# Kernel optimization log

Hardware: AMD Instinct MI355X
Metric: run time of the kernel (lower is better)

Reference implementation:

```python
import jax, jax.numpy as jnp
import numpy as np

EMBED_DIM = 1024
NUM_HEADS = 16
HEAD_DIM = EMBED_DIM // NUM_HEADS


def setup_inputs() -> dict:
    key = jax.random.key(0)
    kx, kw1, kb1, kw2, kb2 = jax.random.split(key, 5)
    B, T, C = 4, 2048, EMBED_DIM
    s = 1.0 / np.sqrt(C)
    return {
        "x": jax.random.normal(kx, (B, T, C), dtype=jnp.float32),
        "qkv_w": jax.random.normal(kw1, (3 * C, C), dtype=jnp.float32) * s,
        "qkv_b": jax.random.normal(kb1, (3 * C,), dtype=jnp.float32) * 0.01,
        "proj_w": jax.random.normal(kw2, (C, C), dtype=jnp.float32) * s,
        "proj_b": jax.random.normal(kb2, (C,), dtype=jnp.float32) * 0.01,
    }


def reference(x, qkv_w, qkv_b, proj_w, proj_b):
    B, T, C = x.shape
    H, D = NUM_HEADS, HEAD_DIM
    qkv = jnp.einsum('btc,oc->bto', x, qkv_w) + qkv_b  # [B,T,3C]
    q, k, v = jnp.split(qkv, 3, axis=-1)
    def heads(t):
        return t.reshape(B, T, H, D).transpose(0, 2, 1, 3)  # [B,H,T,D]
    q, k, v = heads(q), heads(k), heads(v)
    scale = 1.0 / jnp.sqrt(jnp.asarray(D, dtype=x.dtype))
    att = jnp.einsum('bhqd,bhkd->bhqk', q, k) * scale  # [B,H,T,T]
    causal = jnp.tril(jnp.ones((T, T), dtype=bool))
    att = jnp.where(causal, att, -jnp.inf)
    att = jax.nn.softmax(att, axis=-1)
    out = jnp.einsum('bhqk,bhkd->bhqd', att, v)  # [B,H,T,D]
    out = out.transpose(0, 2, 1, 3).reshape(B, T, C)
    out = jnp.einsum('btc,oc->bto', out, proj_w) + proj_b
    return out
```

## Files before the change

### kernel.cpp

```cpp
#include <hip/hip_runtime.h>
#include <hip/hip_bf16.h>

typedef __bf16 bf16x8 __attribute__((ext_vector_type(8)));
typedef __bf16 bf16x4 __attribute__((ext_vector_type(4)));
typedef float  f32x4  __attribute__((ext_vector_type(4)));

#define MFMA16(a, b, c) __builtin_amdgcn_mfma_f32_16x16x32_bf16((a), (b), (c), 0, 0, 0)
#define GLD16(g, l)                                                              \
    __builtin_amdgcn_global_load_lds(                                            \
        (const __attribute__((address_space(1))) void*)(g),                      \
        (__attribute__((address_space(3))) void*)(l), 16, 0, 0)

__global__ __launch_bounds__(256) void cvt3_f32_bf16(const float* __restrict__ a, __bf16* __restrict__ oa, int na,
                                                     const float* __restrict__ b, __bf16* __restrict__ ob, int nb,
                                                     const float* __restrict__ c, __bf16* __restrict__ oc, int nc) {
    const int stride = gridDim.x * blockDim.x * 4;
    const int start = (blockIdx.x * blockDim.x + threadIdx.x) * 4;
    for (int i = start; i < na; i += stride) {
        float4 v = *(const float4*)(a + i);
        bf16x4 o; o[0] = (__bf16)v.x; o[1] = (__bf16)v.y; o[2] = (__bf16)v.z; o[3] = (__bf16)v.w;
        *(bf16x4*)(oa + i) = o;
    }
    for (int i = start; i < nb; i += stride) {
        float4 v = *(const float4*)(b + i);
        bf16x4 o; o[0] = (__bf16)v.x; o[1] = (__bf16)v.y; o[2] = (__bf16)v.z; o[3] = (__bf16)v.w;
        *(bf16x4*)(ob + i) = o;
    }
    for (int i = start; i < nc; i += stride) {
        float4 v = *(const float4*)(c + i);
        bf16x4 o; o[0] = (__bf16)v.x; o[1] = (__bf16)v.y; o[2] = (__bf16)v.z; o[3] = (__bf16)v.w;
        *(bf16x4*)(oc + i) = o;
    }
}

__global__ __launch_bounds__(256, 2) void qkv_gemm(const __bf16* __restrict__ X,
                                                   const __bf16* __restrict__ W,
                                                   const float* __restrict__ bias,
                                                   __bf16* __restrict__ Qo,
                                                   __bf16* __restrict__ Kf,
                                                   __bf16* __restrict__ Vf) {
    const int KD = 1024;
    __shared__ __align__(16) char smem[34816];
    __bf16* As = (__bf16*)smem;
    __bf16* Bs = (__bf16*)(smem + 8192);
    const int tid = threadIdx.x;
    const int lane = tid & 63, w = tid >> 6;
    const int lr = lane & 15, lg = lane >> 4;
    const int orig = blockIdx.x;
    const int wgid = (orig & 7) * 192 + (orig >> 3);
    const int row0 = (wgid & 63) * 128, col0 = (wgid >> 6) * 128;
    const int wrow = (w >> 1) * 64, wcol = (w & 1) * 64;
    f32x4 acc[4][4] = {};
    const int c0 = tid, c1 = tid + 256;
    const __bf16* ga0 = X + (size_t)(row0 + (c0 >> 2)) * KD + (c0 & 3) * 8;
    const __bf16* ga1 = X + (size_t)(row0 + (c1 >> 2)) * KD + (c1 & 3) * 8;
    const __bf16* gb0 = W + (size_t)(col0 + (c0 >> 2)) * KD + (c0 & 3) * 8;
    const __bf16* gb1 = W + (size_t)(col0 + (c1 >> 2)) * KD + (c1 & 3) * 8;
    for (int k0 = 0; k0 < KD; k0 += 32) {
        __syncthreads();
        GLD16(ga0 + k0, As + c0 * 8);
        GLD16(ga1 + k0, As + c1 * 8);
        GLD16(gb0 + k0, Bs + c0 * 8);
        GLD16(gb1 + k0, Bs + c1 * 8);
        __syncthreads();
        bf16x8 a[4], b[4];
#pragma unroll
        for (int mi = 0; mi < 4; mi++)
            a[mi] = *(const bf16x8*)&As[(wrow + mi * 16 + lr) * 32 + lg * 8];
#pragma unroll
        for (int ni = 0; ni < 4; ni++)
            b[ni] = *(const bf16x8*)&Bs[(wcol + ni * 16 + lr) * 32 + lg * 8];
#pragma unroll
        for (int mi = 0; mi < 4; mi++)
#pragma unroll
            for (int ni = 0; ni < 4; ni++)
                acc[mi][ni] = MFMA16(a[mi], b[ni], acc[mi][ni]);
    }

    if (col0 < 1024) {
#pragma unroll
        for (int mi = 0; mi < 4; mi++)
#pragma unroll
            for (int ni = 0; ni < 4; ni++)
#pragma unroll
                for (int r = 0; r < 4; r++) {
                    int m = row0 + wrow + mi * 16 + lg * 4 + r;
                    int n = col0 + wcol + ni * 16 + lr;
                    float v = acc[mi][ni][r] + bias[n];
                    int b_ = m >> 11, t = m & 2047;
                    int c = n & 1023;
                    int bh = b_ * 16 + (c >> 6), d = c & 63;
                    Qo[(size_t)(bh * 2048 + t) * 64 + d] = (__bf16)(v * 0.125f);
                }
    } else if (col0 < 2048) {
#pragma unroll
        for (int mi = 0; mi < 4; mi++)
#pragma unroll
            for (int ni = 0; ni < 4; ni++)
#pragma unroll
                for (int r = 0; r < 4; r++) {
                    int m = row0 + wrow + mi * 16 + lg * 4 + r;
                    int n = col0 + wcol + ni * 16 + lr;
                    float v = acc[mi][ni][r] + bias[n];
                    int b_ = m >> 11, t = m & 2047;
                    int c = n & 1023;
                    int bh = b_ * 16 + (c >> 6), d = c & 63;
                    size_t flat = (((size_t)bh * 128 + (t >> 4)) * 2 + (d >> 5)) * 512
                                + (((d & 31) >> 3) * 16 + (t & 15)) * 8 + (d & 7);
                    Kf[flat] = (__bf16)v;
                }
    } else {
        __syncthreads();
        __bf16* vt = (__bf16*)smem;
#pragma unroll
        for (int mi = 0; mi < 4; mi++)
#pragma unroll
            for (int ni = 0; ni < 4; ni++) {
                int cl = wcol + ni * 16 + lr;
                int tl = wrow + mi * 16 + lg * 4;
                int n = col0 + cl;
                bf16x4 pk;
#pragma unroll
                for (int r = 0; r < 4; r++)
                    pk[r] = (__bf16)(acc[mi][ni][r] + bias[n]);
                *(bf16x4*)&vt[cl * 136 + tl] = pk;
            }
        __syncthreads();
        const int b_ = row0 >> 11, t_base = row0 & 2047;
        const int lane2 = tid & 63, w2 = tid >> 6;
        const int lr2 = lane2 & 15, lg2 = lane2 >> 4;
#pragma unroll
        for (int g = 0; g < 8; g++) {
            int group = g * 4 + w2;
            int hh2 = group >> 4;
            int k32l = (group >> 2) & 3;
            int dt = group & 3;
            const __bf16* src = &vt[(hh2 * 64 + dt * 16 + lr2) * 136 + k32l * 32 + lg2 * 8];
            int c = (col0 & 1023) + hh2 * 64;
            int bh = b_ * 16 + (c >> 6);
            int kt32 = (t_base >> 5) + k32l;
            __bf16* dst = Vf + ((((size_t)bh * 64 + kt32) * 4 + dt) * 512) + lane2 * 8;
            *(bf16x8*)dst = *(const bf16x8*)src;
        }
    }
}

__global__ __launch_bounds__(256) void attn_kernel(const __bf16* __restrict__ Q,
                                                   const __bf16* __restrict__ Kf,
                                                   const __bf16* __restrict__ Vf,
                                                   __bf16* __restrict__ ATT) {
    const int T = 2048, D = 64;
    __shared__ __align__(16) __bf16 plds[4][32][68];
    const int lane = threadIdx.x & 63, w = threadIdx.x >> 6;
    const int lr = lane & 15, lg = lane >> 4;
    const int orig = blockIdx.x;
    const int wgid = (orig & 7) * 64 + (orig >> 3);
    const int bh = wgid >> 3;
    const int idx = (wgid & 7) * 4 + w;
    const int b_ = bh >> 4, hh = bh & 15;
    const __bf16* Qp  = Q  + (size_t)bh * T * D;
    const __bf16* Kfp = Kf + (size_t)bh * 131072;
    const __bf16* Vfp = Vf + (size_t)bh * 131072;

    for (int ph = 0; ph < 2; ++ph) {
        const int j = ph ? 63 - idx : idx;
        const int qrow0 = j * 32;
        bf16x8 qa[2][2];
#pragma unroll
        for (int qt = 0; qt < 2; qt++)
#pragma unroll
            for (int dk = 0; dk < 2; dk++)
                qa[qt][dk] = *(const bf16x8*)(Qp + (size_t)(qrow0 + qt * 16 + lr) * D + dk * 32 + lg * 8);

        float mrow[2][4], lsum[2][4];
#pragma unroll
        for (int qt = 0; qt < 2; qt++)
#pragma unroll
            for (int r = 0; r < 4; r++) { mrow[qt][r] = -1e30f; lsum[qt][r] = 0.f; }
        f32x4 o[2][4] = {};

        const int nkb = (j + 2) >> 1;
        for (int kt0 = 0; kt0 < nkb; ++kt0) {
            const int kb = kt0 * 64;
            bf16x8 kf[4][2];
#pragma unroll
            for (int kt = 0; kt < 4; kt++)
#pragma unroll
                for (int dk = 0; dk < 2; dk++)
                    kf[kt][dk] = *(const bf16x8*)(Kfp + (((kt0 * 4 + kt) * 2 + dk) << 9) + lane * 8);
            f32x4 s[2][4] = {};
#pragma unroll
            for (int qt = 0; qt < 2; qt++)
#pragma unroll
                for (int kt = 0; kt < 4; kt++)
#pragma unroll
                    for (int dk = 0; dk < 2; dk++)
                        s[qt][kt] = MFMA16(qa[qt][dk], kf[kt][dk], s[qt][kt]);

            float lmax[2][4];
            int flag = 0;
#pragma unroll
            for (int qt = 0; qt < 2; qt++)
#pragma unroll
                for (int r = 0; r < 4; r++) {
                    const int qq = qrow0 + qt * 16 + lg * 4 + r;
                    float mt = -1e30f;
#pragma unroll
                    for (int kt = 0; kt < 4; kt++) {
                        float v = (kb + kt * 16 + lr <= qq) ? s[qt][kt][r] : -1e30f;
                        s[qt][kt][r] = v;
                        mt = fmaxf(mt, v);
                    }
                    lmax[qt][r] = mt;
                    flag |= (mt > mrow[qt][r] + 8.0f) ? 1 : 0;
                }

            if (__any(flag)) {
#pragma unroll
                for (int qt = 0; qt < 2; qt++)
#pragma unroll
                    for (int r = 0; r < 4; r++) {
                        float mt = lmax[qt][r];
#pragma unroll
                        for (int off = 1; off < 16; off <<= 1)
                            mt = fmaxf(mt, __shfl_xor(mt, off));
                        float mnew = fmaxf(mrow[qt][r], mt);
                        float al = __expf(mrow[qt][r] - mnew);
                        mrow[qt][r] = mnew;
                        lsum[qt][r] *= al;
#pragma unroll
                        for (int dt = 0; dt < 4; dt++) o[qt][dt][r] *= al;
                    }
            }

#pragma unroll
            for (int qt = 0; qt < 2; qt++)
#pragma unroll
                for (int r = 0; r < 4; r++) {
                    float rs = 0.f;
#pragma unroll
                    for (int kt = 0; kt < 4; kt++) {
                        float p = __expf(s[qt][kt][r] - mrow[qt][r]);
                        s[qt][kt][r] = p;
                        rs += p;
                    }
                    lsum[qt][r] += rs;
                }

#pragma unroll
            for (int qt = 0; qt < 2; qt++)
#pragma unroll
                for (int kt = 0; kt < 4; kt++)
#pragma unroll
                    for (int r = 0; r < 4; r++)
                        plds[w][qt * 16 + lg * 4 + r][kt * 16 + lr] = (__bf16)s[qt][kt][r];

            bf16x8 pa[2][2];
#pragma unroll
            for (int qt = 0; qt < 2; qt++)
#pragma unroll
                for (int kh = 0; kh < 2; kh++)
                    pa[qt][kh] = *(const bf16x8*)&plds[w][qt * 16 + lr][kh * 32 + lg * 8];

#pragma unroll
            for (int kh = 0; kh < 2; kh++) {
                bf16x8 vf[4];
#pragma unroll
                for (int dt = 0; dt < 4; dt++)
                    vf[dt] = *(const bf16x8*)(Vfp + ((((kt0 * 2 + kh) * 4) + dt) << 9) + lane * 8);
#pragma unroll
                for (int qt = 0; qt < 2; qt++)
#pragma unroll
                    for (int dt = 0; dt < 4; dt++)
                        o[qt][dt] = MFMA16(pa[qt][kh], vf[dt], o[qt][dt]);
            }
        }

#pragma unroll
        for (int qt = 0; qt < 2; qt++)
#pragma unroll
            for (int r = 0; r < 4; r++) {
                float rs = lsum[qt][r];
#pragma unroll
                for (int off = 1; off < 16; off <<= 1)
                    rs += __shfl_xor(rs, off);
                lsum[qt][r] = 1.0f / rs;
            }
#pragma unroll
        for (int qt = 0; qt < 2; qt++)
#pragma unroll
            for (int dt = 0; dt < 4; dt++)
#pragma unroll
                for (int r = 0; r < 4; r++) {
                    int qq = qrow0 + qt * 16 + lg * 4 + r;
                    int dd = dt * 16 + lr;
                    float val = o[qt][dt][r] * lsum[qt][r];
                    ATT[(size_t)(b_ * 2048 + qq) * 1024 + hh * 64 + dd] = (__bf16)val;
                }
    }
}

__global__ __launch_bounds__(256, 2) void proj_gemm(const __bf16* __restrict__ A,
                                                    const __bf16* __restrict__ W,
                                                    const float* __restrict__ bias,
                                                    float* __restrict__ out) {
    const int KD = 1024;
    __shared__ __align__(16) __bf16 As[128 * 32];
    __shared__ __align__(16) __bf16 Bs[128 * 32];
    const int tid = threadIdx.x;
    const int lane = tid & 63, w = tid >> 6;
    const int lr = lane & 15, lg = lane >> 4;
    const int orig = blockIdx.x;
    const int wgid = (orig & 7) * 64 + (orig >> 3);
    const int row0 = (wgid & 63) * 128, col0 = (wgid >> 6) * 128;
    const int wrow = (w >> 1) * 64, wcol = (w & 1) * 64;
    f32x4 acc[4][4] = {};
    const int c0 = tid, c1 = tid + 256;
    const __bf16* ga0 = A + (size_t)(row0 + (c0 >> 2)) * KD + (c0 & 3) * 8;
    const __bf16* ga1 = A + (size_t)(row0 + (c1 >> 2)) * KD + (c1 & 3) * 8;
    const __bf16* gb0 = W + (size_t)(col0 + (c0 >> 2)) * KD + (c0 & 3) * 8;
    const __bf16* gb1 = W + (size_t)(col0 + (c1 >> 2)) * KD + (c1 & 3) * 8;
    for (int k0 = 0; k0 < KD; k0 += 32) {
        __syncthreads();
        GLD16(ga0 + k0, As + c0 * 8);
        GLD16(ga1 + k0, As + c1 * 8);
        GLD16(gb0 + k0, Bs + c0 * 8);
        GLD16(gb1 + k0, Bs + c1 * 8);
        __syncthreads();
        bf16x8 a[4], b[4];
#pragma unroll
        for (int mi = 0; mi < 4; mi++)
            a[mi] = *(const bf16x8*)&As[(wrow + mi * 16 + lr) * 32 + lg * 8];
#pragma unroll
        for (int ni = 0; ni < 4; ni++)
            b[ni] = *(const bf16x8*)&Bs[(wcol + ni * 16 + lr) * 32 + lg * 8];
#pragma unroll
        for (int mi = 0; mi < 4; mi++)
#pragma unroll
            for (int ni = 0; ni < 4; ni++)
                acc[mi][ni] = MFMA16(a[mi], b[ni], acc[mi][ni]);
    }
#pragma unroll
    for (int mi = 0; mi < 4; mi++)
#pragma unroll
        for (int ni = 0; ni < 4; ni++)
#pragma unroll
            for (int r = 0; r < 4; r++) {
                int m = row0 + wrow + mi * 16 + lg * 4 + r;
                int n = col0 + wcol + ni * 16 + lr;
                out[(size_t)m * 1024 + n] = acc[mi][ni][r] + bias[n];
            }
}

extern "C" void kernel_launch(void* const* d_in, const int* in_sizes, int n_in,
                              void* d_out, int out_size, void* d_ws, size_t ws_size,
                              hipStream_t stream) {
    const float* x      = (const float*)d_in[0];
    const float* qkv_w  = (const float*)d_in[1];
    const float* qkv_b  = (const float*)d_in[2];
    const float* proj_w = (const float*)d_in[3];
    const float* proj_b = (const float*)d_in[4];
    float* out = (float*)d_out;
    char* ws = (char*)d_ws;

    __bf16* xb    = (__bf16*)(ws);
    __bf16* wqkv  = (__bf16*)(ws + 16777216);
    __bf16* wproj = (__bf16*)(ws + 23068672);
    __bf16* qb    = (__bf16*)(ws + 25165824);
    __bf16* kfb   = (__bf16*)(ws + 41943040);
    __bf16* vfb   = (__bf16*)(ws + 58720256);
    __bf16* attb  = xb;

    cvt3_f32_bf16<<<2048, 256, 0, stream>>>(x, xb, 4 * 2048 * 1024,
                                            qkv_w, wqkv, 3072 * 1024,
                                            proj_w, wproj, 1024 * 1024);
    qkv_gemm<<<1536, 256, 0, stream>>>(xb, wqkv, qkv_b, qb, kfb, vfb);
    attn_kernel<<<512, 256, 0, stream>>>(qb, kfb, vfb, attb);
    proj_gemm<<<512, 256, 0, stream>>>(attb, wproj, proj_b, out);
}
```

Baseline: 191.6 us.

## Split attention KV range across two waves with LDS merge of partial softmax

Attention work is repartitioned. Each 128-thread block now handles one 32-row query tile, and its two waves each process half of the causal key range, like split-K flash decoding. The partial outputs, running maxima and sums are merged through LDS, replacing the earlier scheme where each wave looped over two paired query tiles. This raises the grid from 512 to 4096 blocks to improve load balance and occupancy, at the cost of extra merge work, two block barriers and less K/V reuse per wave.

```diff
diff --git a/kernel.cpp b/kernel.cpp
--- a/kernel.cpp
+++ b/kernel.cpp
@@ -145,158 +145,191 @@
     }
 }
 
-__global__ __launch_bounds__(256) void attn_kernel(const __bf16* __restrict__ Q,
+__global__ __launch_bounds__(128) void attn_kernel(const __bf16* __restrict__ Q,
                                                    const __bf16* __restrict__ Kf,
                                                    const __bf16* __restrict__ Vf,
                                                    __bf16* __restrict__ ATT) {
     const int T = 2048, D = 64;
-    __shared__ __align__(16) __bf16 plds[4][32][68];
+    __shared__ __align__(16) char smem[12544];
     const int lane = threadIdx.x & 63, w = threadIdx.x >> 6;
     const int lr = lane & 15, lg = lane >> 4;
     const int orig = blockIdx.x;
-    const int wgid = (orig & 7) * 64 + (orig >> 3);
-    const int bh = wgid >> 3;
-    const int idx = (wgid & 7) * 4 + w;
+    const int wgid = (orig & 7) * 512 + (orig >> 3);
+    const int bh = wgid >> 6;
+    const int j = 63 - (wgid & 63);
+    const int qrow0 = j * 32;
     const int b_ = bh >> 4, hh = bh & 15;
+    __bf16* plds = (__bf16*)(smem + w * 4352);
+    float*  mbuf = (float*)smem;
     const __bf16* Qp  = Q  + (size_t)bh * T * D;
     const __bf16* Kfp = Kf + (size_t)bh * 131072;
     const __bf16* Vfp = Vf + (size_t)bh * 131072;
 
-    for (int ph = 0; ph < 2; ++ph) {
-        const int j = ph ? 63 - idx : idx;
-        const int qrow0 = j * 32;
-        bf16x8 qa[2][2];
-#pragma unroll
-        for (int qt = 0; qt < 2; qt++)
+    bf16x8 qa[2][2];
+#pragma unroll
+    for (int qt = 0; qt < 2; qt++)
+#pragma unroll
+        for (int dk = 0; dk < 2; dk++)
+            qa[qt][dk] = *(const bf16x8*)(Qp + (size_t)(qrow0 + qt * 16 + lr) * D + dk * 32 + lg * 8);
+
+    float mrow[2][4], lsum[2][4];
+#pragma unroll
+    for (int qt = 0; qt < 2; qt++)
+#pragma unroll
+        for (int r = 0; r < 4; r++) { mrow[qt][r] = -1e30f; lsum[qt][r] = 0.f; }
+    f32x4 o[2][4] = {};
+
+    const int nkb = (j + 2) >> 1;
+    const int mid = nkb >> 1;
+    const int lo = w ? mid : 0;
+    const int hi = w ? nkb : mid;
+    for (int kt0 = lo; kt0 < hi; ++kt0) {
+        const int kb = kt0 * 64;
+        bf16x8 kf[4][2];
+#pragma unroll
+        for (int kt = 0; kt < 4; kt++)
 #pragma unroll
             for (int dk = 0; dk < 2; dk++)
-                qa[qt][dk] = *(const bf16x8*)(Qp + (size_t)(qrow0 + qt * 16 + lr) * D + dk * 32 + lg * 8);
-
-        float mrow[2][4], lsum[2][4];
-#pragma unroll
-        for (int qt = 0; qt < 2; qt++)
-#pragma unroll
-            for (int r = 0; r < 4; r++) { mrow[qt][r] = -1e30f; lsum[qt][r] = 0.f; }
-        f32x4 o[2][4] = {};
-
-        const int nkb = (j + 2) >> 1;
-        for (int kt0 = 0; kt0 < nkb; ++kt0) {
-            const int kb = kt0 * 64;
-            bf16x8 kf[4][2];
+                kf[kt][dk] = *(const bf16x8*)(Kfp + (((kt0 * 4 + kt) * 2 + dk) << 9) + lane * 8);
+        f32x4 s[2][4] = {};
+#pragma unroll
+        for (int qt = 0; qt < 2; qt++)
 #pragma unroll
             for (int kt = 0; kt < 4; kt++)
 #pragma unroll
                 for (int dk = 0; dk < 2; dk++)
-                    kf[kt][dk] = *(const bf16x8*)(Kfp + (((kt0 * 4 + kt) * 2 + dk) << 9) + lane * 8);
-            f32x4 s[2][4] = {};
+                    s[qt][kt] = MFMA16(qa[qt][dk], kf[kt][dk], s[qt][kt]);
+
+        float lmax[2][4];
+        int flag = 0;
+#pragma unroll
+        for (int qt = 0; qt < 2; qt++)
+#pragma unroll
+            for (int r = 0; r < 4; r++) {
+                const int qq = qrow0 + qt * 16 + lg * 4 + r;
+                float mt = -1e30f;
+#pragma unroll
+                for (int kt = 0; kt < 4; kt++) {
+                    float v = (kb + kt * 16 + lr <= qq) ? s[qt][kt][r] : -1e30f;
+                    s[qt][kt][r] = v;
+                    mt = fmaxf(mt, v);
+                }
+                lmax[qt][r] = mt;
+                flag |= (mt > mrow[qt][r] + 8.0f) ? 1 : 0;
+            }
+
+        if (__any(flag)) {
 #pragma unroll
             for (int qt = 0; qt < 2; qt++)
 #pragma unroll
-                for (int kt = 0; kt < 4; kt++)
-#pragma unroll
-                    for (int dk = 0; dk < 2; dk++)
-                        s[qt][kt] = MFMA16(qa[qt][dk], kf[kt][dk], s[qt][kt]);
-
-            float lmax[2][4];
-            int flag = 0;
+                for (int r = 0; r < 4; r++) {
+                    float mt = lmax[qt][r];
+#pragma unroll
+                    for (int off = 1; off < 16; off <<= 1)
+                        mt = fmaxf(mt, __shfl_xor(mt, off));
+                    float mnew = fmaxf(mrow[qt][r], mt);
+                    float al = __expf(mrow[qt][r] - mnew);
+                    mrow[qt][r] = mnew;
+                    lsum[qt][r] *= al;
+#pragma unroll
+                    for (int dt = 0; dt < 4; dt++) o[qt][dt][r] *= al;
+                }
+        }
+
+#pragma unroll
+        for (int qt = 0; qt < 2; qt++)
+#pragma unroll
+            for (int r = 0; r < 4; r++) {
+                float rs = 0.f;
+#pragma unroll
+                for (int kt = 0; kt < 4; kt++) {
+                    float p = __expf(s[qt][kt][r] - mrow[qt][r]);
+                    s[qt][kt][r] = p;
+                    rs += p;
+                }
+                lsum[qt][r] += rs;
+            }
+
+#pragma unroll
+        for (int qt = 0; qt < 2; qt++)
+#pragma unroll
+            for (int kt = 0; kt < 4; kt++)
+#pragma unroll
+                for (int r = 0; r < 4; r++)
+                    plds[(qt * 16 + lg * 4 + r) * 68 + kt * 16 + lr] = (__bf16)s[qt][kt][r];
+
+        bf16x8 pa[2][2];
+#pragma unroll
+        for (int qt = 0; qt < 2; qt++)
+#pragma unroll
+            for (int kh = 0; kh < 2; kh++)
+                pa[qt][kh] = *(const bf16x8*)&plds[(qt * 16 + lr) * 68 + kh * 32 + lg * 8];
+
+#pragma unroll
+        for (int kh = 0; kh < 2; kh++) {
+            bf16x8 vf[4];
+#pragma unroll
+            for (int dt = 0; dt < 4; dt++)
+                vf[dt] = *(const bf16x8*)(Vfp + ((((kt0 * 2 + kh) * 4) + dt) << 9) + lane * 8);
 #pragma unroll
             for (int qt = 0; qt < 2; qt++)
 #pragma unroll
-                for (int r = 0; r < 4; r++) {
-                    const int qq = qrow0 + qt * 16 + lg * 4 + r;
-                    float mt = -1e30f;
-#pragma unroll
-                    for (int kt = 0; kt < 4; kt++) {
-                        float v = (kb + kt * 16 + lr <= qq) ? s[qt][kt][r] : -1e30f;
-                        s[qt][kt][r] = v;
-                        mt = fmaxf(mt, v);
-                    }
-                    lmax[qt][r] = mt;
-                    flag |= (mt > mrow[qt][r] + 8.0f) ? 1 : 0;
-                }
-
-            if (__any(flag)) {
-#pragma unroll
-                for (int qt = 0; qt < 2; qt++)
-#pragma unroll
-                    for (int r = 0; r < 4; r++) {
-                        float mt = lmax[qt][r];
-#pragma unroll
-                        for (int off = 1; off < 16; off <<= 1)
-                            mt = fmaxf(mt, __shfl_xor(mt, off));
-                        float mnew = fmaxf(mrow[qt][r], mt);
-                        float al = __expf(mrow[qt][r] - mnew);
-                        mrow[qt][r] = mnew;
-                        lsum[qt][r] *= al;
-#pragma unroll
-                        for (int dt = 0; dt < 4; dt++) o[qt][dt][r] *= al;
-                    }
-            }
-
-#pragma unroll
-            for (int qt = 0; qt < 2; qt++)
-#pragma unroll
-                for (int r = 0; r < 4; r++) {
-                    float rs = 0.f;
-#pragma unroll
-                    for (int kt = 0; kt < 4; kt++) {
-                        float p = __expf(s[qt][kt][r] - mrow[qt][r]);
-                        s[qt][kt][r] = p;
-                        rs += p;
-                    }
-                    lsum[qt][r] += rs;
-                }
-
-#pragma unroll
-            for (int qt = 0; qt < 2; qt++)
-#pragma unroll
-                for (int kt = 0; kt < 4; kt++)
-#pragma unroll
-                    for (int r = 0; r < 4; r++)
-                        plds[w][qt * 16 + lg * 4 + r][kt * 16 + lr] = (__bf16)s[qt][kt][r];
-
-            bf16x8 pa[2][2];
-#pragma unroll
-            for (int qt = 0; qt < 2; qt++)
-#pragma unroll
-                for (int kh = 0; kh < 2; kh++)
-                    pa[qt][kh] = *(const bf16x8*)&plds[w][qt * 16 + lr][kh * 32 + lg * 8];
-
-#pragma unroll
-            for (int kh = 0; kh < 2; kh++) {
-                bf16x8 vf[4];
-#pragma unroll
                 for (int dt = 0; dt < 4; dt++)
-                    vf[dt] = *(const bf16x8*)(Vfp + ((((kt0 * 2 + kh) * 4) + dt) << 9) + lane * 8);
-#pragma unroll
-                for (int qt = 0; qt < 2; qt++)
-#pragma unroll
-                    for (int dt = 0; dt < 4; dt++)
-                        o[qt][dt] = MFMA16(pa[qt][kh], vf[dt], o[qt][dt]);
-            }
+                    o[qt][dt] = MFMA16(pa[qt][kh], vf[dt], o[qt][dt]);
         }
-
+    }
+
+#pragma unroll
+    for (int qt = 0; qt < 2; qt++)
+#pragma unroll
+        for (int r = 0; r < 4; r++) {
+            float rs = lsum[qt][r];
+#pragma unroll
+            for (int off = 1; off < 16; off <<= 1)
+                rs += __shfl_xor(rs, off);
+            lsum[qt][r] = rs;
+        }
+
+    __syncthreads();
+    if (w == 1) {
+        float* mb = mbuf + lane * 49;
+#pragma unroll
+        for (int qt = 0; qt < 2; qt++)
+#pragma unroll
+            for (int dt = 0; dt < 4; dt++)
+#pragma unroll
+                for (int r = 0; r < 4; r++)
+                    mb[qt * 16 + dt * 4 + r] = o[qt][dt][r];
 #pragma unroll
         for (int qt = 0; qt < 2; qt++)
 #pragma unroll
             for (int r = 0; r < 4; r++) {
-                float rs = lsum[qt][r];
-#pragma unroll
-                for (int off = 1; off < 16; off <<= 1)
-                    rs += __shfl_xor(rs, off);
-                lsum[qt][r] = 1.0f / rs;
-            }
-#pragma unroll
-        for (int qt = 0; qt < 2; qt++)
-#pragma unroll
-            for (int dt = 0; dt < 4; dt++)
-#pragma unroll
-                for (int r = 0; r < 4; r++) {
-                    int qq = qrow0 + qt * 16 + lg * 4 + r;
+                mb[32 + qt * 4 + r] = mrow[qt][r];
+                mb[40 + qt * 4 + r] = lsum[qt][r];
+            }
+    }
+    __syncthreads();
+    if (w == 0) {
+        const float* mb = mbuf + lane * 49;
+#pragma unroll
+        for (int qt = 0; qt < 2; qt++)
+#pragma unroll
+            for (int r = 0; r < 4; r++) {
+                float m1 = mb[32 + qt * 4 + r];
+                float l1 = mb[40 + qt * 4 + r];
+                float m = fmaxf(mrow[qt][r], m1);
+                float a0 = __expf(mrow[qt][r] - m);
+                float a1 = __expf(m1 - m);
+                float inv = 1.0f / (lsum[qt][r] * a0 + l1 * a1);
+                int qq = qrow0 + qt * 16 + lg * 4 + r;
+#pragma unroll
+                for (int dt = 0; dt < 4; dt++) {
                     int dd = dt * 16 + lr;
-                    float val = o[qt][dt][r] * lsum[qt][r];
+                    float v1 = mb[qt * 16 + dt * 4 + r];
+                    float val = (o[qt][dt][r] * a0 + v1 * a1) * inv;
                     ATT[(size_t)(b_ * 2048 + qq) * 1024 + hh * 64 + dd] = (__bf16)val;
                 }
+            }
     }
 }
 
@@ -375,6 +408,6 @@
                                             qkv_w, wqkv, 3072 * 1024,
                                             proj_w, wproj, 1024 * 1024);
     qkv_gemm<<<1536, 256, 0, stream>>>(xb, wqkv, qkv_b, qb, kfb, vfb);
-    attn_kernel<<<512, 256, 0, stream>>>(qb, kfb, vfb, attb);
+    attn_kernel<<<4096, 128, 0, stream>>>(qb, kfb, vfb, attb);
     proj_gemm<<<512, 256, 0, stream>>>(attb, wproj, proj_b, out);
 }
```

After: 217.9 us. 13.7% more time.
